# Optimization experiments

Measured on AMD Instinct MI355X. Metric: run time of the kernel, lower is better.

## Reference

```python
import jax, jax.numpy as jnp
import numpy as np

B, T, X_DIM = 8192, 100, 256
Y_DIM = 6
KSIZE = 50


def setup_inputs() -> dict:
    key = jax.random.key(0)
    k1, k2, k3 = jax.random.split(key, 3)
    sequence = jax.random.normal(k1, (B, T, X_DIM), dtype=jnp.float32)
    # per-feature Conv1d(1,1,k=50,bias=False) weights, stacked as depthwise kernel [X_DIM, 1, K]
    conv_w = jax.random.normal(k2, (X_DIM, 1, KSIZE), dtype=jnp.float32) * 0.1
    # Linear(x_dim -> y_dim*50, bias=False), torch layout [out, in]
    fc_w = jax.random.normal(k3, (Y_DIM * 50, X_DIM), dtype=jnp.float32) * 0.05
    return {"sequence": sequence, "conv_w": conv_w, "fc_w": fc_w}


def reference(sequence, conv_w, fc_w):
    # slice time window 30:100 and move features to channel dim: [B, X_DIM, 70]
    x = jnp.transpose(sequence[:, 30:100, :], (0, 2, 1))
    f = x.shape[1]
    # the Python loop of per-feature Conv1d(1,1,k) ops == one depthwise (grouped) conv
    y = jax.lax.conv_general_dilated(
        x, conv_w,
        window_strides=(1,), padding="VALID",
        dimension_numbers=("NCH", "OIH", "NCH"),
        feature_group_count=f,
    )  # [B, X_DIM, 21]
    # ReLU then max over time -> [B, X_DIM] (kernel_num == 1, so concat == this)
    feat = jnp.max(jax.nn.relu(y), axis=2)
    out = feat @ fc_w.T  # [B, Y_DIM*50]
    return out.reshape(-1, 50, Y_DIM)
```

## Files before the change

### kernel.cpp

```cpp
#include <hip/hip_runtime.h>

#define B_TOTAL 8192
#define T_FULL  100
#define XD      256
#define T0      30
#define TW      70
#define KS      50
#define NT      21
#define YOUT    300
#define FC_NB   16


#define DECLG(G) float G##0,G##1,G##2,G##3,G##4,G##5,G##6,G##7,G##8,G##9;

#define LOADG(G, K0) \
  G##0=xp[(K0+0)*XD]; G##1=xp[(K0+1)*XD]; G##2=xp[(K0+2)*XD]; G##3=xp[(K0+3)*XD]; G##4=xp[(K0+4)*XD]; \
  G##5=xp[(K0+5)*XD]; G##6=xp[(K0+6)*XD]; G##7=xp[(K0+7)*XD]; G##8=xp[(K0+8)*XD]; G##9=xp[(K0+9)*XD];

#define LOADW(K0) \
  w0=wtp[(K0+0)*XD]; w1=wtp[(K0+1)*XD]; w2=wtp[(K0+2)*XD]; w3=wtp[(K0+3)*XD]; w4=wtp[(K0+4)*XD]; \
  w5=wtp[(K0+5)*XD]; w6=wtp[(K0+6)*XD]; w7=wtp[(K0+7)*XD]; w8=wtp[(K0+8)*XD]; w9=wtp[(K0+9)*XD];

#define ROW(A, X0,X1,X2,X3,X4,X5,X6,X7,X8,X9) \
  A=fmaf(X0,w0,A); A=fmaf(X1,w1,A); A=fmaf(X2,w2,A); A=fmaf(X3,w3,A); A=fmaf(X4,w4,A); \
  A=fmaf(X5,w5,A); A=fmaf(X6,w6,A); A=fmaf(X7,w7,A); A=fmaf(X8,w8,A); A=fmaf(X9,w9,A);

#define KB30(y0,y1,y2,y3,y4,y5,y6,y7,y8,y9,y10,y11,y12,y13,y14,y15,y16,y17,y18,y19,y20,y21,y22,y23,y24,y25,y26,y27,y28,y29) \
  ROW(a0 , y0 ,y1 ,y2 ,y3 ,y4 ,y5 ,y6 ,y7 ,y8 ,y9 ) \
  ROW(a1 , y1 ,y2 ,y3 ,y4 ,y5 ,y6 ,y7 ,y8 ,y9 ,y10) \
  ROW(a2 , y2 ,y3 ,y4 ,y5 ,y6 ,y7 ,y8 ,y9 ,y10,y11) \
  ROW(a3 , y3 ,y4 ,y5 ,y6 ,y7 ,y8 ,y9 ,y10,y11,y12) \
  ROW(a4 , y4 ,y5 ,y6 ,y7 ,y8 ,y9 ,y10,y11,y12,y13) \
  ROW(a5 , y5 ,y6 ,y7 ,y8 ,y9 ,y10,y11,y12,y13,y14) \
  ROW(a6 , y6 ,y7 ,y8 ,y9 ,y10,y11,y12,y13,y14,y15) \
  ROW(a7 , y7 ,y8 ,y9 ,y10,y11,y12,y13,y14,y15,y16) \
  ROW(a8 , y8 ,y9 ,y10,y11,y12,y13,y14,y15,y16,y17) \
  ROW(a9 , y9 ,y10,y11,y12,y13,y14,y15,y16,y17,y18) \
  ROW(a10, y10,y11,y12,y13,y14,y15,y16,y17,y18,y19) \
  ROW(a11, y11,y12,y13,y14,y15,y16,y17,y18,y19,y20) \
  ROW(a12, y12,y13,y14,y15,y16,y17,y18,y19,y20,y21) \
  ROW(a13, y13,y14,y15,y16,y17,y18,y19,y20,y21,y22) \
  ROW(a14, y14,y15,y16,y17,y18,y19,y20,y21,y22,y23) \
  ROW(a15, y15,y16,y17,y18,y19,y20,y21,y22,y23,y24) \
  ROW(a16, y16,y17,y18,y19,y20,y21,y22,y23,y24,y25) \
  ROW(a17, y17,y18,y19,y20,y21,y22,y23,y24,y25,y26) \
  ROW(a18, y18,y19,y20,y21,y22,y23,y24,y25,y26,y27) \
  ROW(a19, y19,y20,y21,y22,y23,y24,y25,y26,y27,y28) \
  ROW(a20, y20,y21,y22,y23,y24,y25,y26,y27,y28,y29)

#define KB30X(...) KB30(__VA_ARGS__)

#define GA xa0,xa1,xa2,xa3,xa4,xa5,xa6,xa7,xa8,xa9
#define GB xb0,xb1,xb2,xb3,xb4,xb5,xb6,xb7,xb8,xb9
#define GC xc0,xc1,xc2,xc3,xc4,xc5,xc6,xc7,xc8,xc9
#define GD xd0,xd1,xd2,xd3,xd4,xd5,xd6,xd7,xd8,xd9

__global__ __launch_bounds__(256)
void transpose_w(const float* __restrict__ conv_w, const float* __restrict__ fc_w,
                 float* __restrict__ wt, float* __restrict__ fct) {
    const int i = blockIdx.x * 256 + threadIdx.x;
    if (i < XD * KS) {
        const int f = i / KS;
        const int k = i - f * KS;
        wt[k * XD + f] = conv_w[i];
    }
    if (i < YOUT * XD) {
        const int o = i >> 8;
        const int q = i & 255;
        fct[q * YOUT + o] = fc_w[i];
    }
}

__global__ __launch_bounds__(256, 4)
void conv_kernel(const float* __restrict__ seq, const float* __restrict__ wt,
                 float* __restrict__ feat) {
    const int f = threadIdx.x;
    const int b = blockIdx.x;
    const float* xp  = seq + ((size_t)b * T_FULL + T0) * XD + f;
    const float* wtp = wt + f;

    float a0=0,a1=0,a2=0,a3=0,a4=0,a5=0,a6=0,a7=0,a8=0,a9=0,a10=0,
          a11=0,a12=0,a13=0,a14=0,a15=0,a16=0,a17=0,a18=0,a19=0,a20=0;
    DECLG(xa) DECLG(xb) DECLG(xc) DECLG(xd)
    float w0,w1,w2,w3,w4,w5,w6,w7,w8,w9;

    LOADW(0);  LOADG(xa, 0) LOADG(xb, 10) LOADG(xc, 20)
    KB30X(GA, GB, GC)
    LOADG(xd, 30) LOADW(10);
    KB30X(GB, GC, GD)
    LOADG(xa, 40) LOADW(20);
    KB30X(GC, GD, GA)
    LOADG(xb, 50) LOADW(30);
    KB30X(GD, GA, GB)
    LOADG(xc, 60) LOADW(40);
    KB30X(GA, GB, GC)

    float m = 0.f;
    m=fmaxf(m,a0 ); m=fmaxf(m,a1 ); m=fmaxf(m,a2 ); m=fmaxf(m,a3 ); m=fmaxf(m,a4 );
    m=fmaxf(m,a5 ); m=fmaxf(m,a6 ); m=fmaxf(m,a7 ); m=fmaxf(m,a8 ); m=fmaxf(m,a9 );
    m=fmaxf(m,a10); m=fmaxf(m,a11); m=fmaxf(m,a12); m=fmaxf(m,a13); m=fmaxf(m,a14);
    m=fmaxf(m,a15); m=fmaxf(m,a16); m=fmaxf(m,a17); m=fmaxf(m,a18); m=fmaxf(m,a19);
    m=fmaxf(m,a20);
    feat[(size_t)b * XD + f] = m;
}

#define FCSTEP(C, NB_) C = fmaf(wv, fb[(NB_) * XD + q], C);

__global__ __launch_bounds__(320, 2)
void fc_kernel(const float* __restrict__ feat, const float* __restrict__ fct,
               float* __restrict__ out) {
    const int o  = threadIdx.x;
    const int b0 = blockIdx.x * FC_NB;
    if (o >= YOUT) return;

    const float* fb = feat + (size_t)b0 * XD;

    float c0=0,c1=0,c2=0,c3=0,c4=0,c5=0,c6=0,c7=0,
          c8=0,c9=0,c10=0,c11=0,c12=0,c13=0,c14=0,c15=0;

#pragma unroll 2
    for (int q = 0; q < XD; ++q) {
        const float wv = fct[q * YOUT + o];
        FCSTEP(c0 , 0)  FCSTEP(c1 , 1)  FCSTEP(c2 , 2)  FCSTEP(c3 , 3)
        FCSTEP(c4 , 4)  FCSTEP(c5 , 5)  FCSTEP(c6 , 6)  FCSTEP(c7 , 7)
        FCSTEP(c8 , 8)  FCSTEP(c9 , 9)  FCSTEP(c10,10)  FCSTEP(c11,11)
        FCSTEP(c12,12)  FCSTEP(c13,13)  FCSTEP(c14,14)  FCSTEP(c15,15)
    }

    out[(size_t)(b0 +  0) * YOUT + o] = c0;
    out[(size_t)(b0 +  1) * YOUT + o] = c1;
    out[(size_t)(b0 +  2) * YOUT + o] = c2;
    out[(size_t)(b0 +  3) * YOUT + o] = c3;
    out[(size_t)(b0 +  4) * YOUT + o] = c4;
    out[(size_t)(b0 +  5) * YOUT + o] = c5;
    out[(size_t)(b0 +  6) * YOUT + o] = c6;
    out[(size_t)(b0 +  7) * YOUT + o] = c7;
    out[(size_t)(b0 +  8) * YOUT + o] = c8;
    out[(size_t)(b0 +  9) * YOUT + o] = c9;
    out[(size_t)(b0 + 10) * YOUT + o] = c10;
    out[(size_t)(b0 + 11) * YOUT + o] = c11;
    out[(size_t)(b0 + 12) * YOUT + o] = c12;
    out[(size_t)(b0 + 13) * YOUT + o] = c13;
    out[(size_t)(b0 + 14) * YOUT + o] = c14;
    out[(size_t)(b0 + 15) * YOUT + o] = c15;
}

extern "C" void kernel_launch(void* const* d_in, const int* in_sizes, int n_in,
                              void* d_out, int out_size, void* d_ws, size_t ws_size,
                              hipStream_t stream) {
    const float* seq    = (const float*)d_in[0];
    const float* conv_w = (const float*)d_in[1];
    const float* fc_w   = (const float*)d_in[2];
    float*       out    = (float*)d_out;

    float* wt   = (float*)d_ws;
    float* fct  = wt  + XD * KS;
    float* feat = fct + XD * YOUT;

    transpose_w<<<dim3((YOUT * XD + 255) / 256), dim3(256), 0, stream>>>(conv_w, fc_w, wt, fct);
    conv_kernel<<<dim3(B_TOTAL), dim3(256), 0, stream>>>(seq, wt, feat);
    fc_kernel<<<dim3(B_TOTAL / FC_NB), dim3(320), 0, stream>>>(feat, fct, out);
}
```

Before: 184.0 us.

## Stream conv input through LDS via async global_load_lds with manual vmcnt pipelining

The conv kernel now loads its sequence window with global_load_lds, which writes straight into per-wave LDS ring slots. It keeps up to four 10-row chunks in flight and waits on them with hand-placed s_waitcnt vmcnt barriers before reading each chunk back from LDS. Weights are double-buffered in two register sets so the next weight chunk loads while the current one is used. The goal is deeper memory-level parallelism and overlap of loads with FMA work. The cost is 40KB of LDS per block, which may limit occupancy, plus fragile manual waitcnt counting that the compiler's own scheduling could invalidate.

```diff
diff --git a/kernel.cpp b/kernel.cpp
--- a/kernel.cpp
+++ b/kernel.cpp
@@ -13,40 +13,54 @@
 
 #define DECLG(G) float G##0,G##1,G##2,G##3,G##4,G##5,G##6,G##7,G##8,G##9;
 
-#define LOADG(G, K0) \
-  G##0=xp[(K0+0)*XD]; G##1=xp[(K0+1)*XD]; G##2=xp[(K0+2)*XD]; G##3=xp[(K0+3)*XD]; G##4=xp[(K0+4)*XD]; \
-  G##5=xp[(K0+5)*XD]; G##6=xp[(K0+6)*XD]; G##7=xp[(K0+7)*XD]; G##8=xp[(K0+8)*XD]; G##9=xp[(K0+9)*XD];
+#define VMF(N) asm volatile("s_waitcnt vmcnt(" #N ")" ::: "memory")
 
-#define LOADW(K0) \
-  w0=wtp[(K0+0)*XD]; w1=wtp[(K0+1)*XD]; w2=wtp[(K0+2)*XD]; w3=wtp[(K0+3)*XD]; w4=wtp[(K0+4)*XD]; \
-  w5=wtp[(K0+5)*XD]; w6=wtp[(K0+6)*XD]; w7=wtp[(K0+7)*XD]; w8=wtp[(K0+8)*XD]; w9=wtp[(K0+9)*XD];
+#define GLL1(c, s, r) \
+  __builtin_amdgcn_global_load_lds( \
+      (const __attribute__((address_space(1))) void*)(xp + ((c)*10 + (r)) * XD), \
+      (__attribute__((address_space(3))) void*)(ldsr + (s)*640 + (r)*64), 4, 0, 0);
 
-#define ROW(A, X0,X1,X2,X3,X4,X5,X6,X7,X8,X9) \
-  A=fmaf(X0,w0,A); A=fmaf(X1,w1,A); A=fmaf(X2,w2,A); A=fmaf(X3,w3,A); A=fmaf(X4,w4,A); \
-  A=fmaf(X5,w5,A); A=fmaf(X6,w6,A); A=fmaf(X7,w7,A); A=fmaf(X8,w8,A); A=fmaf(X9,w9,A);
+#define GLL(c, s) \
+  GLL1(c,s,0) GLL1(c,s,1) GLL1(c,s,2) GLL1(c,s,3) GLL1(c,s,4) \
+  GLL1(c,s,5) GLL1(c,s,6) GLL1(c,s,7) GLL1(c,s,8) GLL1(c,s,9)
 
-#define KB30(y0,y1,y2,y3,y4,y5,y6,y7,y8,y9,y10,y11,y12,y13,y14,y15,y16,y17,y18,y19,y20,y21,y22,y23,y24,y25,y26,y27,y28,y29) \
-  ROW(a0 , y0 ,y1 ,y2 ,y3 ,y4 ,y5 ,y6 ,y7 ,y8 ,y9 ) \
-  ROW(a1 , y1 ,y2 ,y3 ,y4 ,y5 ,y6 ,y7 ,y8 ,y9 ,y10) \
-  ROW(a2 , y2 ,y3 ,y4 ,y5 ,y6 ,y7 ,y8 ,y9 ,y10,y11) \
-  ROW(a3 , y3 ,y4 ,y5 ,y6 ,y7 ,y8 ,y9 ,y10,y11,y12) \
-  ROW(a4 , y4 ,y5 ,y6 ,y7 ,y8 ,y9 ,y10,y11,y12,y13) \
-  ROW(a5 , y5 ,y6 ,y7 ,y8 ,y9 ,y10,y11,y12,y13,y14) \
-  ROW(a6 , y6 ,y7 ,y8 ,y9 ,y10,y11,y12,y13,y14,y15) \
-  ROW(a7 , y7 ,y8 ,y9 ,y10,y11,y12,y13,y14,y15,y16) \
-  ROW(a8 , y8 ,y9 ,y10,y11,y12,y13,y14,y15,y16,y17) \
-  ROW(a9 , y9 ,y10,y11,y12,y13,y14,y15,y16,y17,y18) \
-  ROW(a10, y10,y11,y12,y13,y14,y15,y16,y17,y18,y19) \
-  ROW(a11, y11,y12,y13,y14,y15,y16,y17,y18,y19,y20) \
-  ROW(a12, y12,y13,y14,y15,y16,y17,y18,y19,y20,y21) \
-  ROW(a13, y13,y14,y15,y16,y17,y18,y19,y20,y21,y22) \
-  ROW(a14, y14,y15,y16,y17,y18,y19,y20,y21,y22,y23) \
-  ROW(a15, y15,y16,y17,y18,y19,y20,y21,y22,y23,y24) \
-  ROW(a16, y16,y17,y18,y19,y20,y21,y22,y23,y24,y25) \
-  ROW(a17, y17,y18,y19,y20,y21,y22,y23,y24,y25,y26) \
-  ROW(a18, y18,y19,y20,y21,y22,y23,y24,y25,y26,y27) \
-  ROW(a19, y19,y20,y21,y22,y23,y24,y25,y26,y27,y28) \
-  ROW(a20, y20,y21,y22,y23,y24,y25,y26,y27,y28,y29)
+#define LOADL(G, s) \
+  G##0=ldsr[(s)*640+  0+lane]; G##1=ldsr[(s)*640+ 64+lane]; \
+  G##2=ldsr[(s)*640+128+lane]; G##3=ldsr[(s)*640+192+lane]; \
+  G##4=ldsr[(s)*640+256+lane]; G##5=ldsr[(s)*640+320+lane]; \
+  G##6=ldsr[(s)*640+384+lane]; G##7=ldsr[(s)*640+448+lane]; \
+  G##8=ldsr[(s)*640+512+lane]; G##9=ldsr[(s)*640+576+lane];
+
+#define LOADWSET(W, K0) \
+  W##0=wtp[(K0+0)*XD]; W##1=wtp[(K0+1)*XD]; W##2=wtp[(K0+2)*XD]; W##3=wtp[(K0+3)*XD]; W##4=wtp[(K0+4)*XD]; \
+  W##5=wtp[(K0+5)*XD]; W##6=wtp[(K0+6)*XD]; W##7=wtp[(K0+7)*XD]; W##8=wtp[(K0+8)*XD]; W##9=wtp[(K0+9)*XD];
+
+#define ROW(A, W, X0,X1,X2,X3,X4,X5,X6,X7,X8,X9) \
+  A=fmaf(X0,W##0,A); A=fmaf(X1,W##1,A); A=fmaf(X2,W##2,A); A=fmaf(X3,W##3,A); A=fmaf(X4,W##4,A); \
+  A=fmaf(X5,W##5,A); A=fmaf(X6,W##6,A); A=fmaf(X7,W##7,A); A=fmaf(X8,W##8,A); A=fmaf(X9,W##9,A);
+
+#define KB30(W, y0,y1,y2,y3,y4,y5,y6,y7,y8,y9,y10,y11,y12,y13,y14,y15,y16,y17,y18,y19,y20,y21,y22,y23,y24,y25,y26,y27,y28,y29) \
+  ROW(a0 , W, y0 ,y1 ,y2 ,y3 ,y4 ,y5 ,y6 ,y7 ,y8 ,y9 ) \
+  ROW(a1 , W, y1 ,y2 ,y3 ,y4 ,y5 ,y6 ,y7 ,y8 ,y9 ,y10) \
+  ROW(a2 , W, y2 ,y3 ,y4 ,y5 ,y6 ,y7 ,y8 ,y9 ,y10,y11) \
+  ROW(a3 , W, y3 ,y4 ,y5 ,y6 ,y7 ,y8 ,y9 ,y10,y11,y12) \
+  ROW(a4 , W, y4 ,y5 ,y6 ,y7 ,y8 ,y9 ,y10,y11,y12,y13) \
+  ROW(a5 , W, y5 ,y6 ,y7 ,y8 ,y9 ,y10,y11,y12,y13,y14) \
+  ROW(a6 , W, y6 ,y7 ,y8 ,y9 ,y10,y11,y12,y13,y14,y15) \
+  ROW(a7 , W, y7 ,y8 ,y9 ,y10,y11,y12,y13,y14,y15,y16) \
+  ROW(a8 , W, y8 ,y9 ,y10,y11,y12,y13,y14,y15,y16,y17) \
+  ROW(a9 , W, y9 ,y10,y11,y12,y13,y14,y15,y16,y17,y18) \
+  ROW(a10, W, y10,y11,y12,y13,y14,y15,y16,y17,y18,y19) \
+  ROW(a11, W, y11,y12,y13,y14,y15,y16,y17,y18,y19,y20) \
+  ROW(a12, W, y12,y13,y14,y15,y16,y17,y18,y19,y20,y21) \
+  ROW(a13, W, y13,y14,y15,y16,y17,y18,y19,y20,y21,y22) \
+  ROW(a14, W, y14,y15,y16,y17,y18,y19,y20,y21,y22,y23) \
+  ROW(a15, W, y15,y16,y17,y18,y19,y20,y21,y22,y23,y24) \
+  ROW(a16, W, y16,y17,y18,y19,y20,y21,y22,y23,y24,y25) \
+  ROW(a17, W, y17,y18,y19,y20,y21,y22,y23,y24,y25,y26) \
+  ROW(a18, W, y18,y19,y20,y21,y22,y23,y24,y25,y26,y27) \
+  ROW(a19, W, y19,y20,y21,y22,y23,y24,y25,y26,y27,y28) \
+  ROW(a20, W, y20,y21,y22,y23,y24,y25,y26,y27,y28,y29)
 
 #define KB30X(...) KB30(__VA_ARGS__)
 
@@ -74,26 +88,39 @@
 __global__ __launch_bounds__(256, 4)
 void conv_kernel(const float* __restrict__ seq, const float* __restrict__ wt,
                  float* __restrict__ feat) {
-    const int f = threadIdx.x;
-    const int b = blockIdx.x;
-    const float* xp  = seq + ((size_t)b * T_FULL + T0) * XD + f;
-    const float* wtp = wt + f;
+    __shared__ float lds[4 * 4 * 640];
+    const int lane = threadIdx.x & 63;
+    const int wv   = threadIdx.x >> 6;
+    const int b    = blockIdx.x;
+    const float* xp  = seq + ((size_t)b * T_FULL + T0) * XD + threadIdx.x;
+    const float* wtp = wt + threadIdx.x;
+    float* ldsr = &lds[wv * 2560];
 
     float a0=0,a1=0,a2=0,a3=0,a4=0,a5=0,a6=0,a7=0,a8=0,a9=0,a10=0,
           a11=0,a12=0,a13=0,a14=0,a15=0,a16=0,a17=0,a18=0,a19=0,a20=0;
     DECLG(xa) DECLG(xb) DECLG(xc) DECLG(xd)
-    float w0,w1,w2,w3,w4,w5,w6,w7,w8,w9;
+    DECLG(wa) DECLG(wb)
 
-    LOADW(0);  LOADG(xa, 0) LOADG(xb, 10) LOADG(xc, 20)
-    KB30X(GA, GB, GC)
-    LOADG(xd, 30) LOADW(10);
-    KB30X(GB, GC, GD)
-    LOADG(xa, 40) LOADW(20);
-    KB30X(GC, GD, GA)
-    LOADG(xb, 50) LOADW(30);
-    KB30X(GD, GA, GB)
-    LOADG(xc, 60) LOADW(40);
-    KB30X(GA, GB, GC)
+    GLL(0,0) GLL(1,1) GLL(2,2) GLL(3,3)
+    LOADWSET(wa, 0); LOADWSET(wb, 10);
+    VMF(50);  LOADL(xa, 0)
+    VMF(40);  LOADL(xb, 1)
+    GLL(4,0)
+    VMF(30);  LOADL(xc, 2)
+    KB30X(wa, GA, GB, GC)
+    LOADWSET(wa, 20);
+    GLL(5,1)
+    VMF(50);  LOADL(xd, 3)
+    KB30X(wb, GB, GC, GD)
+    LOADWSET(wb, 30);
+    GLL(6,2)
+    VMF(40);  LOADL(xa, 0)
+    KB30X(wa, GC, GD, GA)
+    LOADWSET(wa, 40);
+    VMF(30);  LOADL(xb, 1)
+    KB30X(wb, GD, GA, GB)
+    VMF(10);  LOADL(xc, 2)
+    KB30X(wa, GA, GB, GC)
 
     float m = 0.f;
     m=fmaxf(m,a0 ); m=fmaxf(m,a1 ); m=fmaxf(m,a2 ); m=fmaxf(m,a3 ); m=fmaxf(m,a4 );
@@ -101,10 +128,10 @@
     m=fmaxf(m,a10); m=fmaxf(m,a11); m=fmaxf(m,a12); m=fmaxf(m,a13); m=fmaxf(m,a14);
     m=fmaxf(m,a15); m=fmaxf(m,a16); m=fmaxf(m,a17); m=fmaxf(m,a18); m=fmaxf(m,a19);
     m=fmaxf(m,a20);
-    feat[(size_t)b * XD + f] = m;
+    feat[(size_t)b * XD + threadIdx.x] = m;
 }
 
-#define FCSTEP(C, NB_) C = fmaf(wv, fb[(NB_) * XD + q], C);
+#define FCSTEP(C, NB_) C = fmaf(wv_, fb[(NB_) * XD + q], C);
 
 __global__ __launch_bounds__(320, 2)
 void fc_kernel(const float* __restrict__ feat, const float* __restrict__ fct,
@@ -120,7 +147,7 @@
 
 #pragma unroll 2
     for (int q = 0; q < XD; ++q) {
-        const float wv = fct[q * YOUT + o];
+        const float wv_ = fct[q * YOUT + o];
         FCSTEP(c0 , 0)  FCSTEP(c1 , 1)  FCSTEP(c2 , 2)  FCSTEP(c3 , 3)
         FCSTEP(c4 , 4)  FCSTEP(c5 , 5)  FCSTEP(c6 , 6)  FCSTEP(c7 , 7)
         FCSTEP(c8 , 8)  FCSTEP(c9 , 9)  FCSTEP(c10,10)  FCSTEP(c11,11)
```

Result: no change. 184.9 us (+0.5%).
